# Kernel tuning notes

Hardware: AMD Instinct MI355X
Metric: run time of the kernel (lower is better)

The kernel has to match this reference:

```python
import jax, jax.numpy as jnp
import numpy as np
import math

B, T, C = 4, 1024, 1024
H = 16          # n_head
E = 8           # num_experts
K = 2           # top_k
HID = 4096      # expert_hidden_dim
TEMP = 1.0
EPS_LN = 1e-5


def setup_inputs() -> dict:
    key = jax.random.key(0)
    ks = jax.random.split(key, 16)
    s = 0.02
    return {
        'x': jax.random.normal(ks[0], (B, T, C), jnp.float32),
        'ln1_g': jnp.ones((C,), jnp.float32),
        'ln1_b': jnp.zeros((C,), jnp.float32),
        'W_qkv': jax.random.normal(ks[1], (C, 3 * C), jnp.float32) * s,
        'b_qkv': jnp.zeros((3 * C,), jnp.float32),
        'W_proj': jax.random.normal(ks[2], (C, C), jnp.float32) * s,
        'b_proj': jnp.zeros((C,), jnp.float32),
        'ln2_g': jnp.ones((C,), jnp.float32),
        'ln2_b': jnp.zeros((C,), jnp.float32),
        'W_router': jax.random.normal(ks[3], (C, E), jnp.float32) * s,
        'W1': jax.random.normal(ks[4], (E, C, HID), jnp.float32) * s,
        'b1': jnp.zeros((E, HID), jnp.float32),
        'W2': jax.random.normal(ks[5], (E, HID, C), jnp.float32) * s,
        'b2': jnp.zeros((E, C), jnp.float32),
    }


def _layernorm(x, g, b):
    mu = jnp.mean(x, axis=-1, keepdims=True)
    var = jnp.mean(jnp.square(x - mu), axis=-1, keepdims=True)
    return (x - mu) * jax.lax.rsqrt(var + EPS_LN) * g + b


def reference(x, ln1_g, ln1_b, W_qkv, b_qkv, W_proj, b_proj,
              ln2_g, ln2_b, W_router, W1, b1, W2, b2):
    D = C // H
    # --- causal self-attention on ln_1(x) ---
    h = _layernorm(x, ln1_g, ln1_b)
    qkv = h @ W_qkv + b_qkv                      # [B,T,3C]
    q, k, v = jnp.split(qkv, 3, axis=-1)
    q = q.reshape(B, T, H, D).transpose(0, 2, 1, 3)   # [B,H,T,D]
    k = k.reshape(B, T, H, D).transpose(0, 2, 1, 3)
    v = v.reshape(B, T, H, D).transpose(0, 2, 1, 3)
    att = jnp.einsum('bhqd,bhkd->bhqk', q, k) * (1.0 / math.sqrt(D))
    mask = jnp.tril(jnp.ones((T, T), bool))
    att = jnp.where(mask, att, -jnp.inf)
    att = jax.nn.softmax(att, axis=-1)
    y = jnp.einsum('bhqk,bhkd->bhqd', att, v)
    y = y.transpose(0, 2, 1, 3).reshape(B, T, C)
    x = x + (y @ W_proj + b_proj)

    # --- sparse MoE on ln_2(x) ---
    h2 = _layernorm(x, ln2_g, ln2_b)
    xf = h2.reshape(-1, C)                       # [N,C]
    N = xf.shape[0]
    logits = (xf @ W_router) / TEMP              # [N,E]
    prob = jax.nn.softmax(logits, axis=-1)
    top_prob, top_idx = jax.lax.top_k(prob, K)   # [N,K]
    top_prob = top_prob / (jnp.sum(top_prob, axis=-1, keepdims=True) + 1e-9)
    # dense per-token per-expert combine weights (0 for unselected experts)
    w = jnp.zeros((N, E), xf.dtype).at[jnp.arange(N)[:, None], top_idx].add(top_prob)
    # dense expert compute (weights zero out unselected experts -> same math)
    hid = jax.nn.gelu(jnp.einsum('nc,ech->neh', xf, W1) + b1, approximate=False)
    eo = jnp.einsum('neh,ehc->nec', hid, W2) + b2          # [N,E,C]
    out_flat = jnp.einsum('nec,ne->nc', eo, w)
    x = x + out_flat.reshape(B, T, C)

    counts = jnp.zeros((E,), jnp.float32).at[top_idx.reshape(-1)].add(1.0)
    expert_utilization = counts / (jnp.sum(counts) + 1e-9)
    return x, expert_utilization
```

## Files before the change

### kernel.cpp

```cpp
#include <hip/hip_runtime.h>
#include <cmath>

#define CDIM 1024
#define NTOK 4096
#define NHEAD 16
#define HDIM 64
#define NEXP 8
#define HIDD 4096
#define MAXROWS 9216

typedef short bf16x8 __attribute__((ext_vector_type(8)));
typedef short s16x4  __attribute__((ext_vector_type(4)));
typedef float f32x4  __attribute__((ext_vector_type(4)));

static __device__ __forceinline__ short f2bf(float f){
  unsigned u = __builtin_bit_cast(unsigned, f);
  u += 0x7fffu + ((u >> 16) & 1u);
  return (short)(u >> 16);
}

static __device__ __forceinline__ int swz64(int r, int ch){
  return r*64 + (((ch ^ (r>>1)) & 3) << 4);
}
static __device__ __forceinline__ int swz128(int r, int ch){
  return r*128 + (((ch ^ r) & 7) << 4);
}

__global__ void k_transpose_cast(const float* __restrict__ in, short* __restrict__ out,
                                 int R, int Cc){
  __shared__ float tile[32][33];
  const int z = blockIdx.z;
  const float* src = in + (long long)z*R*Cc;
  short* dst = out + (long long)z*R*Cc;
  const int c  = blockIdx.x*32 + threadIdx.x;
  const int r0 = blockIdx.y*32;
  #pragma unroll
  for (int i=0;i<4;i++)
    tile[threadIdx.y + i*8][threadIdx.x] = src[(long long)(r0 + threadIdx.y + i*8)*Cc + c];
  __syncthreads();
  const int rr = r0 + threadIdx.x;
  #pragma unroll
  for (int i=0;i<4;i++){
    int cc = blockIdx.x*32 + threadIdx.y + i*8;
    dst[(long long)cc*R + rr] = f2bf(tile[threadIdx.x][threadIdx.y + i*8]);
  }
}

__global__ void k_ln1(const float* __restrict__ x, const float* __restrict__ g,
                      const float* __restrict__ b, short* __restrict__ out){
  const int row = blockIdx.x;
  const int t = threadIdx.x;
  const float4 v = ((const float4*)(x + (long long)row*CDIM))[t];
  float s  = v.x+v.y+v.z+v.w;
  float s2 = v.x*v.x+v.y*v.y+v.z*v.z+v.w*v.w;
  #pragma unroll
  for (int mm=1; mm<64; mm<<=1){ s += __shfl_xor(s,mm); s2 += __shfl_xor(s2,mm); }
  __shared__ float ps[4], ps2[4];
  const int w = t>>6, l = t&63;
  if (l==0){ ps[w]=s; ps2[w]=s2; }
  __syncthreads();
  s  = ps[0]+ps[1]+ps[2]+ps[3];
  s2 = ps2[0]+ps2[1]+ps2[2]+ps2[3];
  const float mu = s*(1.f/CDIM);
  const float rstd = rsqrtf(s2*(1.f/CDIM) - mu*mu + 1e-5f);
  const float4 gg = ((const float4*)g)[t];
  const float4 bb = ((const float4*)b)[t];
  s16x4 o;
  o[0]=f2bf((v.x-mu)*rstd*gg.x+bb.x); o[1]=f2bf((v.y-mu)*rstd*gg.y+bb.y);
  o[2]=f2bf((v.z-mu)*rstd*gg.z+bb.z); o[3]=f2bf((v.w-mu)*rstd*gg.w+bb.w);
  *(s16x4*)(out + (long long)row*CDIM + t*4) = o;
}

__global__ void k_ln2_router(const float* __restrict__ x1, const float* __restrict__ g,
                             const float* __restrict__ b, const float* __restrict__ Wr,
                             short* __restrict__ h2, int* __restrict__ tidx,
                             float* __restrict__ tw, int* __restrict__ counts){
  const int row = blockIdx.x;
  const int t = threadIdx.x;
  const float4 v = ((const float4*)(x1 + (long long)row*CDIM))[t];
  float s  = v.x+v.y+v.z+v.w;
  float s2 = v.x*v.x+v.y*v.y+v.z*v.z+v.w*v.w;
  #pragma unroll
  for (int mm=1; mm<64; mm<<=1){ s += __shfl_xor(s,mm); s2 += __shfl_xor(s2,mm); }
  __shared__ float ps[4], ps2[4];
  const int w = t>>6, l = t&63;
  if (l==0){ ps[w]=s; ps2[w]=s2; }
  __syncthreads();
  s  = ps[0]+ps[1]+ps[2]+ps[3];
  s2 = ps2[0]+ps2[1]+ps2[2]+ps2[3];
  const float mu = s*(1.f/CDIM);
  const float rstd = rsqrtf(s2*(1.f/CDIM) - mu*mu + 1e-5f);
  const float4 gg = ((const float4*)g)[t];
  const float4 bb = ((const float4*)b)[t];
  const float y0=(v.x-mu)*rstd*gg.x+bb.x, y1=(v.y-mu)*rstd*gg.y+bb.y;
  const float y2=(v.z-mu)*rstd*gg.z+bb.z, y3=(v.w-mu)*rstd*gg.w+bb.w;
  s16x4 o; o[0]=f2bf(y0); o[1]=f2bf(y1); o[2]=f2bf(y2); o[3]=f2bf(y3);
  *(s16x4*)(h2 + (long long)row*CDIM + t*4) = o;

  float acc[8];
  const float* wr0 = Wr + (long long)(t*4)*NEXP;
  #pragma unroll
  for (int e=0;e<8;e++) acc[e] = y0*wr0[e] + y1*wr0[8+e] + y2*wr0[16+e] + y3*wr0[24+e];
  #pragma unroll
  for (int mm=1; mm<64; mm<<=1){
    #pragma unroll
    for (int e=0;e<8;e++) acc[e] += __shfl_xor(acc[e], mm);
  }
  __shared__ float pl[4][8];
  if (l==0){
    #pragma unroll
    for (int e=0;e<8;e++) pl[w][e]=acc[e];
  }
  __syncthreads();
  if (t==0){
    float lg[8];
    #pragma unroll
    for (int e=0;e<8;e++) lg[e] = pl[0][e]+pl[1][e]+pl[2][e]+pl[3][e];
    float mx = lg[0];
    #pragma unroll
    for (int e=1;e<8;e++) mx = fmaxf(mx, lg[e]);
    float pr[8]; float sum = 0.f;
    #pragma unroll
    for (int e=0;e<8;e++){ pr[e]=expf(lg[e]-mx); sum += pr[e]; }
    int i0 = 0;
    #pragma unroll
    for (int e=1;e<8;e++) if (pr[e] > pr[i0]) i0 = e;
    int i1 = (i0==0) ? 1 : 0;
    #pragma unroll
    for (int e=0;e<8;e++) if (e!=i0 && pr[e] > pr[i1]) i1 = e;
    const float p0 = pr[i0]/sum, p1 = pr[i1]/sum;
    const float dn = p0 + p1 + 1e-9f;
    tidx[row*2]=i0; tidx[row*2+1]=i1;
    tw[row*2]=p0/dn; tw[row*2+1]=p1/dn;
    atomicAdd(&counts[i0],1); atomicAdd(&counts[i1],1);
  }
}

__global__ void k_route_setup(const int* __restrict__ counts, int* __restrict__ offs,
                              int* __restrict__ cursors, int* __restrict__ rowmap,
                              float* __restrict__ util){
  if (threadIdx.x == 0){
    int o = 0;
    for (int e=0;e<8;e++){
      offs[e] = o; cursors[e] = o;
      o += (counts[e] + 127) & ~127;
    }
    offs[8] = o;
    for (int e=0;e<8;e++) util[e] = (float)counts[e] / 8192.0f;
  }
  for (int i = threadIdx.x; i < MAXROWS; i += blockDim.x) rowmap[i] = -1;
}

__global__ void k_scatter(const int* __restrict__ tidx, const float* __restrict__ tw,
                          int* __restrict__ cursors, int* __restrict__ rowmap,
                          float* __restrict__ roww, int* __restrict__ posmap){
  const int i = blockIdx.x*blockDim.x + threadIdx.x;
  if (i >= 2*NTOK) return;
  const int e = tidx[i];
  const int pos = atomicAdd(&cursors[e], 1);
  rowmap[pos] = i >> 1;
  roww[pos]   = tw[i];
  posmap[i]   = pos;
}

template<int EPI>
__launch_bounds__(256)
__global__ void k_gemm(const short* __restrict__ A, const short* __restrict__ Bt,
                       const float* __restrict__ bias, const float* __restrict__ resid,
                       void* __restrict__ Cout, int N, int K,
                       const int* __restrict__ rowmap, const int* __restrict__ offs,
                       long long expStrideB){
  const int mbase = blockIdx.x*128;
  const int nbase = blockIdx.y*128;
  int e = 0;
  if constexpr (EPI >= 2){
    if (mbase >= offs[8]) return;
    while (e < 7 && mbase >= offs[e+1]) e++;
    Bt += (long long)e * expStrideB;
  }
  __shared__ short Asm[128*32];
  __shared__ short Bsm[128*32];
  const int tid = threadIdx.x;
  const int w = tid >> 6, l = tid & 63;
  const int wr = w >> 1, wc = w & 1;
  const int l15 = l & 15, l4 = l >> 4;

  f32x4 acc[4][4];
  const f32x4 z4 = {0.f,0.f,0.f,0.f};
  #pragma unroll
  for (int i=0;i<4;i++){
    #pragma unroll
    for (int jn=0;jn<4;jn++) acc[i][jn] = z4;
  }

  for (int kt = 0; kt < K; kt += 32){
    #pragma unroll
    for (int p=0;p<2;p++){
      const int ch = tid + p*256;
      const int r = ch >> 2, c4 = ch & 3;
      bf16x8 va;
      if constexpr (EPI == 2){
        const int grow = rowmap[mbase + r];
        #pragma unroll
        for (int q=0;q<8;q++) va[q] = 0;
        if (grow >= 0) va = *(const bf16x8*)(A + (long long)grow*K + kt + c4*8);
      } else {
        va = *(const bf16x8*)(A + (long long)(mbase + r)*K + kt + c4*8);
      }
      *(bf16x8*)((char*)Asm + swz64(r, c4)) = va;
      bf16x8 vb = *(const bf16x8*)(Bt + (long long)(nbase + r)*K + kt + c4*8);
      *(bf16x8*)((char*)Bsm + swz64(r, c4)) = vb;
    }
    __syncthreads();
    bf16x8 af[4], bfr[4];
    #pragma unroll
    for (int i=0;i<4;i++){
      af[i]  = *(const bf16x8*)((char*)Asm + swz64(wr*64 + i*16 + l15, l4));
      bfr[i] = *(const bf16x8*)((char*)Bsm + swz64(wc*64 + i*16 + l15, l4));
    }
    #pragma unroll
    for (int i=0;i<4;i++){
      #pragma unroll
      for (int jn=0;jn<4;jn++)
        acc[i][jn] = __builtin_amdgcn_mfma_f32_16x16x32_bf16(af[i], bfr[jn], acc[i][jn], 0,0,0);
    }
    __syncthreads();
  }

  #pragma unroll
  for (int i=0;i<4;i++){
    const int row0 = mbase + wr*64 + i*16 + l4*4;
    #pragma unroll
    for (int jn=0;jn<4;jn++){
      const int col = nbase + wc*64 + jn*16 + l15;
      const float bi = bias[(EPI>=2 ? e*N : 0) + col];
      #pragma unroll
      for (int j=0;j<4;j++){
        const long long idx = (long long)(row0 + j)*N + col;
        float v = acc[i][jn][j] + bi;
        if constexpr (EPI == 0){
          ((short*)Cout)[idx] = f2bf(v);
        } else if constexpr (EPI == 1){
          ((float*)Cout)[idx] = v + resid[idx];
        } else if constexpr (EPI == 2){
          ((short*)Cout)[idx] = f2bf(0.5f*v*(1.0f + erff(v*0.70710678118654752f)));
        } else {
          ((float*)Cout)[idx] = v;
        }
      }
    }
  }
}

__launch_bounds__(256)
__global__ void k_attn(const short* __restrict__ qkv, short* __restrict__ y){
  const int qt = blockIdx.x;
  const int bh = blockIdx.y;
  const int bb = bh >> 4;
  const int h  = bh & 15;
  const int tid = threadIdx.x;
  const int w = tid >> 6, l = tid & 63;
  const int l15 = l & 15, l4 = l >> 4;

  __shared__ short Ksm[64*64];
  __shared__ short Vtsm[64*64];
  __shared__ short Psm[4*16*64];

  const long long rs = 3*CDIM;
  const int qrow0 = bb*1024 + qt*64;

  bf16x8 aq[2];
  {
    const int qr = qrow0 + w*16 + l15;
    const short* qp = qkv + (long long)qr*rs + h*HDIM;
    aq[0] = *(const bf16x8*)(qp + l4*8);
    aq[1] = *(const bf16x8*)(qp + 32 + l4*8);
  }

  const f32x4 z4 = {0.f,0.f,0.f,0.f};
  f32x4 O[4];
  #pragma unroll
  for (int cf=0;cf<4;cf++) O[cf] = z4;
  float mrow[4], lrow[4];
  #pragma unroll
  for (int j=0;j<4;j++){ mrow[j] = -1e30f; lrow[j] = 0.f; }

  for (int kvb = 0; kvb <= qt; ++kvb){
    const int kvrow0 = bb*1024 + kvb*64;
    #pragma unroll
    for (int p=0;p<2;p++){
      const int ch = tid + p*256;
      const int r = ch >> 3, c = ch & 7;
      const short* kp = qkv + (long long)(kvrow0 + r)*rs + CDIM + h*HDIM + c*8;
      *(bf16x8*)((char*)Ksm + swz128(r, c)) = *(const bf16x8*)kp;
      const short* vp = qkv + (long long)(kvrow0 + r)*rs + 2*CDIM + h*HDIM + c*8;
      bf16x8 vv = *(const bf16x8*)vp;
      const int off2 = 2*r;
      const int g0 = off2 >> 4, b0 = off2 & 15;
      #pragma unroll
      for (int i=0;i<8;i++){
        const int d = c*8 + i;
        *(short*)((char*)Vtsm + d*128 + (((g0 ^ d) & 7) << 4) + b0) = vv[i];
      }
    }
    __syncthreads();

    f32x4 S[4];
    #pragma unroll
    for (int cf=0;cf<4;cf++) S[cf] = z4;
    #pragma unroll
    for (int cf=0;cf<4;cf++){
      #pragma unroll
      for (int kf=0;kf<2;kf++){
        bf16x8 bk = *(const bf16x8*)((char*)Ksm + swz128(cf*16 + l15, kf*4 + l4));
        S[cf] = __builtin_amdgcn_mfma_f32_16x16x32_bf16(aq[kf], bk, S[cf], 0,0,0);
      }
    }

    const bool diag = (kvb == qt);
    #pragma unroll
    for (int cf=0;cf<4;cf++){
      #pragma unroll
      for (int j=0;j<4;j++){
        float s = S[cf][j] * 0.125f;
        if (diag && (cf*16 + l15 > w*16 + l4*4 + j)) s = -1e30f;
        S[cf][j] = s;
      }
    }

    float alpha[4];
    #pragma unroll
    for (int j=0;j<4;j++){
      float mx = fmaxf(fmaxf(S[0][j],S[1][j]), fmaxf(S[2][j],S[3][j]));
      #pragma unroll
      for (int mm=1; mm<16; mm<<=1) mx = fmaxf(mx, __shfl_xor(mx, mm));
      const float mnew = fmaxf(mrow[j], mx);
      const float al = expf(mrow[j] - mnew);
      float psum = 0.f;
      #pragma unroll
      for (int cf=0;cf<4;cf++){ float pp = expf(S[cf][j]-mnew); S[cf][j]=pp; psum += pp; }
      #pragma unroll
      for (int mm=1; mm<16; mm<<=1) psum += __shfl_xor(psum, mm);
      lrow[j] = lrow[j]*al + psum;
      mrow[j] = mnew; alpha[j] = al;
    }
    #pragma unroll
    for (int cf=0;cf<4;cf++){
      #pragma unroll
      for (int j=0;j<4;j++) O[cf][j] *= alpha[j];
    }

    char* pw = (char*)Psm + w*2048;
    #pragma unroll
    for (int cf=0;cf<4;cf++){
      #pragma unroll
      for (int j=0;j<4;j++){
        const int r = l4*4 + j;
        const int cb = (cf*16 + l15)*2;
        *(short*)(pw + r*128 + ((((cb>>4) ^ r) & 7)<<4) + (cb & 15)) = f2bf(S[cf][j]);
      }
    }
    bf16x8 pa[2];
    pa[0] = *(const bf16x8*)(pw + swz128(l15, l4));
    pa[1] = *(const bf16x8*)(pw + swz128(l15, 4 + l4));
    #pragma unroll
    for (int cf=0;cf<4;cf++){
      #pragma unroll
      for (int kf=0;kf<2;kf++){
        bf16x8 bv = *(const bf16x8*)((char*)Vtsm + swz128(cf*16 + l15, kf*4 + l4));
        O[cf] = __builtin_amdgcn_mfma_f32_16x16x32_bf16(pa[kf], bv, O[cf], 0,0,0);
      }
    }
    __syncthreads();
  }

  const int yr0 = qrow0 + w*16;
  #pragma unroll
  for (int cf=0;cf<4;cf++){
    #pragma unroll
    for (int j=0;j<4;j++){
      const int r = l4*4 + j;
      y[(long long)(yr0 + r)*CDIM + h*HDIM + cf*16 + l15] = f2bf(O[cf][j] / lrow[j]);
    }
  }
}

__global__ void k_combine(const float* __restrict__ x1, const float* __restrict__ eo,
                          const int* __restrict__ posmap, const float* __restrict__ roww,
                          float* __restrict__ out){
  const int row = blockIdx.x;
  const int t = threadIdx.x;
  const int p0 = posmap[row*2], p1 = posmap[row*2+1];
  const float w0 = roww[p0], w1 = roww[p1];
  const float4 a  = ((const float4*)(x1 + (long long)row*CDIM))[t];
  const float4 e0 = ((const float4*)(eo + (long long)p0*CDIM))[t];
  const float4 e1 = ((const float4*)(eo + (long long)p1*CDIM))[t];
  float4 r;
  r.x = a.x + w0*e0.x + w1*e1.x;
  r.y = a.y + w0*e0.y + w1*e1.y;
  r.z = a.z + w0*e0.z + w1*e1.z;
  r.w = a.w + w0*e0.w + w1*e1.w;
  ((float4*)(out + (long long)row*CDIM))[t] = r;
}

extern "C" void kernel_launch(void* const* d_in, const int* in_sizes, int n_in,
                              void* d_out, int out_size, void* d_ws, size_t ws_size,
                              hipStream_t stream){
  const float* x     = (const float*)d_in[0];
  const float* ln1_g = (const float*)d_in[1];
  const float* ln1_b = (const float*)d_in[2];
  const float* W_qkv = (const float*)d_in[3];
  const float* b_qkv = (const float*)d_in[4];
  const float* W_proj= (const float*)d_in[5];
  const float* b_proj= (const float*)d_in[6];
  const float* ln2_g = (const float*)d_in[7];
  const float* ln2_b = (const float*)d_in[8];
  const float* W_r   = (const float*)d_in[9];
  const float* W1    = (const float*)d_in[10];
  const float* b1    = (const float*)d_in[11];
  const float* W2    = (const float*)d_in[12];
  const float* b2    = (const float*)d_in[13];
  float* out = (float*)d_out;
  float* util = out + (long long)NTOK*CDIM;

  char* p = (char*)d_ws;
  auto alloc = [&](size_t bytes)->char*{
    char* r = p; p += (bytes + 255) & ~(size_t)255; return r;
  };
  short* Wt1   = (short*)alloc((size_t)NEXP*HIDD*CDIM*2);
  short* Wt2   = (short*)alloc((size_t)NEXP*CDIM*HIDD*2);
  float* x1    = (float*)alloc((size_t)NTOK*CDIM*4);
  short* h2    = (short*)alloc((size_t)NTOK*CDIM*2);
  short* hid   = (short*)alloc((size_t)MAXROWS*HIDD*2);
  int*   tidx  = (int*)alloc(2*NTOK*4);
  float* tw    = (float*)alloc(2*NTOK*4);
  int*   counts= (int*)alloc(256);
  int*   offs  = (int*)alloc(256);
  int*   curs  = (int*)alloc(256);
  int*   rowmap= (int*)alloc(MAXROWS*4);
  float* roww  = (float*)alloc(MAXROWS*4);
  int*   posmap= (int*)alloc(2*NTOK*4);
  char* transStart = p;
  short* WtQ = (short*)alloc((size_t)3*CDIM*CDIM*2);
  short* WtP = (short*)alloc((size_t)CDIM*CDIM*2);
  short* h   = (short*)alloc((size_t)NTOK*CDIM*2);
  short* qkv = (short*)alloc((size_t)NTOK*3*CDIM*2);
  short* y   = (short*)alloc((size_t)NTOK*CDIM*2);
  float* eo  = (float*)transStart;

  dim3 tb(32,8);
  k_transpose_cast<<<dim3(3*CDIM/32, CDIM/32, 1), tb, 0, stream>>>(W_qkv, WtQ, CDIM, 3*CDIM);
  k_transpose_cast<<<dim3(CDIM/32, CDIM/32, 1),   tb, 0, stream>>>(W_proj, WtP, CDIM, CDIM);
  k_transpose_cast<<<dim3(HIDD/32, CDIM/32, NEXP),tb, 0, stream>>>(W1, Wt1, CDIM, HIDD);
  k_transpose_cast<<<dim3(CDIM/32, HIDD/32, NEXP),tb, 0, stream>>>(W2, Wt2, HIDD, CDIM);

  k_ln1<<<NTOK, 256, 0, stream>>>(x, ln1_g, ln1_b, h);

  k_gemm<0><<<dim3(NTOK/128, 3*CDIM/128), 256, 0, stream>>>(
      h, WtQ, b_qkv, nullptr, qkv, 3*CDIM, CDIM, nullptr, nullptr, 0);

  k_attn<<<dim3(1024/64, 4*NHEAD), 256, 0, stream>>>(qkv, y);

  k_gemm<1><<<dim3(NTOK/128, CDIM/128), 256, 0, stream>>>(
      y, WtP, b_proj, x, x1, CDIM, CDIM, nullptr, nullptr, 0);

  (void)hipMemsetAsync(counts, 0, 32, stream);
  k_ln2_router<<<NTOK, 256, 0, stream>>>(x1, ln2_g, ln2_b, W_r, h2, tidx, tw, counts);
  k_route_setup<<<1, 256, 0, stream>>>(counts, offs, curs, rowmap, util);
  k_scatter<<<(2*NTOK)/256, 256, 0, stream>>>(tidx, tw, curs, rowmap, roww, posmap);

  k_gemm<2><<<dim3(MAXROWS/128, HIDD/128), 256, 0, stream>>>(
      h2, Wt1, b1, nullptr, hid, HIDD, CDIM, rowmap, offs, (long long)HIDD*CDIM);
  k_gemm<3><<<dim3(MAXROWS/128, CDIM/128), 256, 0, stream>>>(
      hid, Wt2, b2, nullptr, eo, CDIM, HIDD, nullptr, offs, (long long)CDIM*HIDD);

  k_combine<<<NTOK, 256, 0, stream>>>(x1, eo, posmap, roww, out);
}
```

Measured before the change: 722.5 us.

## Use direct global-to-LDS loads, XCD-aware tile remap, and vectorized weight transpose

The GEMM staging now uses global_load_lds intrinsics that copy 16-byte chunks straight into pre-swizzled shared memory, bypassing registers. Gathered rows that are unused read from a zeroed buffer instead of taking a branch. Workgroup IDs are remapped to a 1D grid so consecutive tiles land on the same XCD, which should improve L2 reuse. The weight transpose-cast kernel moves to 64x64 tiles with float4 loads and 16-byte bf16 stores, cutting per-call weight conversion cost. A new zero-row buffer and a reordered memset are added.

```diff
diff --git a/kernel.cpp b/kernel.cpp
--- a/kernel.cpp
+++ b/kernel.cpp
@@ -26,23 +26,36 @@
   return r*128 + (((ch ^ r) & 7) << 4);
 }
 
+static __device__ __forceinline__ void gl16(const short* g, short* l){
+  __builtin_amdgcn_global_load_lds(
+      (const __attribute__((address_space(1))) void*)g,
+      (__attribute__((address_space(3))) void*)l, 16, 0, 0);
+}
+
 __global__ void k_transpose_cast(const float* __restrict__ in, short* __restrict__ out,
                                  int R, int Cc){
-  __shared__ float tile[32][33];
+  __shared__ float tile[64][65];
   const int z = blockIdx.z;
   const float* src = in + (long long)z*R*Cc;
   short* dst = out + (long long)z*R*Cc;
-  const int c  = blockIdx.x*32 + threadIdx.x;
-  const int r0 = blockIdx.y*32;
-  #pragma unroll
-  for (int i=0;i<4;i++)
-    tile[threadIdx.y + i*8][threadIdx.x] = src[(long long)(r0 + threadIdx.y + i*8)*Cc + c];
+  const int r0 = blockIdx.y*64, c0 = blockIdx.x*64;
+  const int t = threadIdx.x;
+  #pragma unroll
+  for (int it=0; it<4; ++it){
+    const int item = t + it*256;
+    const int r = item>>4, c4 = item&15;
+    const float4 v = *(const float4*)(src + (long long)(r0+r)*Cc + c0 + c4*4);
+    tile[r][c4*4+0]=v.x; tile[r][c4*4+1]=v.y; tile[r][c4*4+2]=v.z; tile[r][c4*4+3]=v.w;
+  }
   __syncthreads();
-  const int rr = r0 + threadIdx.x;
-  #pragma unroll
-  for (int i=0;i<4;i++){
-    int cc = blockIdx.x*32 + threadIdx.y + i*8;
-    dst[(long long)cc*R + rr] = f2bf(tile[threadIdx.x][threadIdx.y + i*8]);
+  #pragma unroll
+  for (int it=0; it<2; ++it){
+    const int item = t + it*256;
+    const int rr8 = item & 7, cc = item >> 3;
+    bf16x8 o;
+    #pragma unroll
+    for (int i=0;i<8;i++) o[i] = f2bf(tile[rr8*8+i][cc]);
+    *(bf16x8*)(dst + (long long)(c0+cc)*R + r0 + rr8*8) = o;
   }
 }
 
@@ -169,9 +182,19 @@
                        const float* __restrict__ bias, const float* __restrict__ resid,
                        void* __restrict__ Cout, int N, int K,
                        const int* __restrict__ rowmap, const int* __restrict__ offs,
-                       long long expStrideB){
-  const int mbase = blockIdx.x*128;
-  const int nbase = blockIdx.y*128;
+                       long long expStrideB, const short* __restrict__ zrow){
+  int wg = blockIdx.x;
+  const int nwg = gridDim.x;
+  {
+    const int q = nwg >> 3, r8 = nwg & 7;
+    const int xcd = wg & 7, pos = wg >> 3;
+    wg = (xcd < r8 ? xcd*(q+1) : r8*(q+1) + (xcd - r8)*q) + pos;
+  }
+  const int gridN = N >> 7;
+  const int gridM = nwg / gridN;
+  const int mtile = wg % gridM, ntile = wg / gridM;
+  const int mbase = mtile*128;
+  const int nbase = ntile*128;
   int e = 0;
   if constexpr (EPI >= 2){
     if (mbase >= offs[8]) return;
@@ -185,6 +208,24 @@
   const int wr = w >> 1, wc = w & 1;
   const int l15 = l & 15, l4 = l >> 4;
 
+  const short* aSrc[2]; const short* bSrc[2];
+  short* aDst[2]; short* bDst[2];
+  #pragma unroll
+  for (int inst=0; inst<2; ++inst){
+    const int g = w*128 + inst*64 + l;
+    const int r = g >> 2, ch = g & 3;
+    const int sch = (ch ^ (r >> 1)) & 3;
+    if constexpr (EPI == 2){
+      const int grow = rowmap[mbase + r];
+      aSrc[inst] = (grow >= 0) ? (A + (long long)grow*K + sch*8) : (zrow + sch*8);
+    } else {
+      aSrc[inst] = A + (long long)(mbase + r)*K + sch*8;
+    }
+    bSrc[inst] = Bt + (long long)(nbase + r)*K + sch*8;
+    aDst[inst] = Asm + w*1024 + inst*512;
+    bDst[inst] = Bsm + w*1024 + inst*512;
+  }
+
   f32x4 acc[4][4];
   const f32x4 z4 = {0.f,0.f,0.f,0.f};
   #pragma unroll
@@ -195,21 +236,9 @@
 
   for (int kt = 0; kt < K; kt += 32){
     #pragma unroll
-    for (int p=0;p<2;p++){
-      const int ch = tid + p*256;
-      const int r = ch >> 2, c4 = ch & 3;
-      bf16x8 va;
-      if constexpr (EPI == 2){
-        const int grow = rowmap[mbase + r];
-        #pragma unroll
-        for (int q=0;q<8;q++) va[q] = 0;
-        if (grow >= 0) va = *(const bf16x8*)(A + (long long)grow*K + kt + c4*8);
-      } else {
-        va = *(const bf16x8*)(A + (long long)(mbase + r)*K + kt + c4*8);
-      }
-      *(bf16x8*)((char*)Asm + swz64(r, c4)) = va;
-      bf16x8 vb = *(const bf16x8*)(Bt + (long long)(nbase + r)*K + kt + c4*8);
-      *(bf16x8*)((char*)Bsm + swz64(r, c4)) = vb;
+    for (int inst=0; inst<2; ++inst){
+      gl16(aSrc[inst] + kt, aDst[inst]);
+      gl16(bSrc[inst] + kt, bDst[inst]);
     }
     __syncthreads();
     bf16x8 af[4], bfr[4];
@@ -440,6 +469,7 @@
   int*   rowmap= (int*)alloc(MAXROWS*4);
   float* roww  = (float*)alloc(MAXROWS*4);
   int*   posmap= (int*)alloc(2*NTOK*4);
+  short* zrow  = (short*)alloc(8192);
   char* transStart = p;
   short* WtQ = (short*)alloc((size_t)3*CDIM*CDIM*2);
   short* WtP = (short*)alloc((size_t)CDIM*CDIM*2);
@@ -448,31 +478,32 @@
   short* y   = (short*)alloc((size_t)NTOK*CDIM*2);
   float* eo  = (float*)transStart;
 
-  dim3 tb(32,8);
-  k_transpose_cast<<<dim3(3*CDIM/32, CDIM/32, 1), tb, 0, stream>>>(W_qkv, WtQ, CDIM, 3*CDIM);
-  k_transpose_cast<<<dim3(CDIM/32, CDIM/32, 1),   tb, 0, stream>>>(W_proj, WtP, CDIM, CDIM);
-  k_transpose_cast<<<dim3(HIDD/32, CDIM/32, NEXP),tb, 0, stream>>>(W1, Wt1, CDIM, HIDD);
-  k_transpose_cast<<<dim3(CDIM/32, HIDD/32, NEXP),tb, 0, stream>>>(W2, Wt2, HIDD, CDIM);
+  (void)hipMemsetAsync(counts, 0, 32, stream);
+  (void)hipMemsetAsync(zrow, 0, 8192, stream);
+
+  k_transpose_cast<<<dim3(3*CDIM/64, CDIM/64, 1), 256, 0, stream>>>(W_qkv, WtQ, CDIM, 3*CDIM);
+  k_transpose_cast<<<dim3(CDIM/64, CDIM/64, 1),   256, 0, stream>>>(W_proj, WtP, CDIM, CDIM);
+  k_transpose_cast<<<dim3(HIDD/64, CDIM/64, NEXP),256, 0, stream>>>(W1, Wt1, CDIM, HIDD);
+  k_transpose_cast<<<dim3(CDIM/64, HIDD/64, NEXP),256, 0, stream>>>(W2, Wt2, HIDD, CDIM);
 
   k_ln1<<<NTOK, 256, 0, stream>>>(x, ln1_g, ln1_b, h);
 
-  k_gemm<0><<<dim3(NTOK/128, 3*CDIM/128), 256, 0, stream>>>(
-      h, WtQ, b_qkv, nullptr, qkv, 3*CDIM, CDIM, nullptr, nullptr, 0);
+  k_gemm<0><<<dim3((NTOK/128)*(3*CDIM/128)), 256, 0, stream>>>(
+      h, WtQ, b_qkv, nullptr, qkv, 3*CDIM, CDIM, nullptr, nullptr, 0, nullptr);
 
   k_attn<<<dim3(1024/64, 4*NHEAD), 256, 0, stream>>>(qkv, y);
 
-  k_gemm<1><<<dim3(NTOK/128, CDIM/128), 256, 0, stream>>>(
-      y, WtP, b_proj, x, x1, CDIM, CDIM, nullptr, nullptr, 0);
-
-  (void)hipMemsetAsync(counts, 0, 32, stream);
+  k_gemm<1><<<dim3((NTOK/128)*(CDIM/128)), 256, 0, stream>>>(
+      y, WtP, b_proj, x, x1, CDIM, CDIM, nullptr, nullptr, 0, nullptr);
+
   k_ln2_router<<<NTOK, 256, 0, stream>>>(x1, ln2_g, ln2_b, W_r, h2, tidx, tw, counts);
   k_route_setup<<<1, 256, 0, stream>>>(counts, offs, curs, rowmap, util);
   k_scatter<<<(2*NTOK)/256, 256, 0, stream>>>(tidx, tw, curs, rowmap, roww, posmap);
 
-  k_gemm<2><<<dim3(MAXROWS/128, HIDD/128), 256, 0, stream>>>(
-      h2, Wt1, b1, nullptr, hid, HIDD, CDIM, rowmap, offs, (long long)HIDD*CDIM);
-  k_gemm<3><<<dim3(MAXROWS/128, CDIM/128), 256, 0, stream>>>(
-      hid, Wt2, b2, nullptr, eo, CDIM, HIDD, nullptr, offs, (long long)CDIM*HIDD);
+  k_gemm<2><<<dim3((MAXROWS/128)*(HIDD/128)), 256, 0, stream>>>(
+      h2, Wt1, b1, nullptr, hid, HIDD, CDIM, rowmap, offs, (long long)HIDD*CDIM, zrow);
+  k_gemm<3><<<dim3((MAXROWS/128)*(CDIM/128)), 256, 0, stream>>>(
+      hid, Wt2, b2, nullptr, eo, CDIM, HIDD, nullptr, offs, (long long)CDIM*HIDD, zrow);
 
   k_combine<<<NTOK, 256, 0, stream>>>(x1, eo, posmap, roww, out);
 }
```

Result: faster. 698.0 us (-3.4%).
